# Kernel tuning notes

Measured on AMD Instinct MI355X. Metric: run time of the kernel, lower is better.

## Reference

```python
import jax, jax.numpy as jnp
import numpy as np

B, S, D, F, E = 8, 4096, 512, 2048, 8
INIT_LAMBDA = 0.2
LN_EPS = 1e-5
LN_MERGE = 0.03  # scale used when merging layer_norm expert task-vectors


def setup_inputs() -> dict:
    key = jax.random.key(0)
    ks = jax.random.split(key, 12)
    n = lambda k, shp, s=1.0: jax.random.normal(k, shp, dtype=jnp.float32) * s
    return {
        "hidden_states": n(ks[0], (B, S, D)),
        # DictMoEGate (2 hidden layers): fc1 ~ N(0, 0.01), fc2 bias = init_lambda
        "gfc1_w": n(ks[1], (D, D), 0.01),
        "gfc1_b": jnp.zeros((D,), jnp.float32),
        "gfc2_w": n(ks[2], (E, D), 0.01),
        "gfc2_b": jnp.full((E,), INIT_LAMBDA, dtype=jnp.float32),
        # base PositionWiseFeedForward params (torch Linear layout: [out, in])
        "W1": n(ks[3], (F, D), 0.02),
        "b1": jnp.zeros((F,), jnp.float32),
        "W2": n(ks[4], (D, F), 0.02),
        "b2": jnp.zeros((D,), jnp.float32),
        "ln_g": jnp.ones((D,), jnp.float32),
        "ln_b": jnp.zeros((D,), jnp.float32),
        # expert task vectors (expert_sd - base_sd), one per base param
        "tv_W1": n(ks[5], (E, F, D), 0.02),
        "tv_b1": n(ks[6], (E, F), 0.02),
        "tv_W2": n(ks[7], (E, D, F), 0.02),
        "tv_b2": n(ks[8], (E, D), 0.02),
        "tv_ln_g": n(ks[9], (E, D), 0.02),
        "tv_ln_b": n(ks[10], (E, D), 0.02),
    }


def reference(hidden_states, gfc1_w, gfc1_b, gfc2_w, gfc2_b,
              W1, b1, W2, b2, ln_g, ln_b,
              tv_W1, tv_b1, tv_W2, tv_b2, tv_ln_g, tv_ln_b):
    x = hidden_states  # [B, S, D] (batch_first)
    # --- gate: per-token 2-layer MLP, then mean over sequence -> [B, E] ---
    gh = jax.nn.relu(jnp.einsum('bsd,hd->bsh', x, gfc1_w) + gfc1_b)
    g = (jnp.einsum('bsh,eh->bse', gh, gfc2_w) + gfc2_b).mean(axis=1)  # [B, E]
    # --- per-sample merged weights: base + sum_e g[b,e] * task_vector[e] ---
    W1m = W1 + jnp.einsum('be,efd->bfd', g, tv_W1)   # [B, F, D]
    b1m = b1 + g @ tv_b1                              # [B, F]
    W2m = W2 + jnp.einsum('be,edf->bdf', g, tv_W2)   # [B, D, F]
    b2m = b2 + g @ tv_b2                              # [B, D]
    # layer_norm params: sd = param + sum_e (tv_e - param) * 0.03 (gate-independent)
    lng = ln_g + LN_MERGE * (tv_ln_g - ln_g).sum(axis=0)  # [D]
    lnb = ln_b + LN_MERGE * (tv_ln_b - ln_b).sum(axis=0)  # [D]
    # --- PositionWiseFeedForward with per-sample weights (dropout = eval/identity) ---
    h = jax.nn.relu(jnp.einsum('bsd,bfd->bsf', x, W1m) + b1m[:, None, :])  # [B, S, F]
    out = jnp.einsum('bsf,bdf->bsd', h, W2m) + b2m[:, None, :]             # [B, S, D]
    res = x + out
    mu = res.mean(axis=-1, keepdims=True)
    var = res.var(axis=-1, keepdims=True)
    return (res - mu) * jax.lax.rsqrt(var + LN_EPS) * lng + lnb
```

## Files before the change

kernel.cpp:

```cpp
#include <hip/hip_runtime.h>

typedef __bf16 bf16;
typedef __attribute__((ext_vector_type(4))) __bf16 bf16x4;
typedef __attribute__((ext_vector_type(8))) __bf16 bf16x8;
typedef __attribute__((ext_vector_type(4))) float f32x4;

#define LDS16(gp, lp)                                                          \
  __builtin_amdgcn_global_load_lds(                                            \
      (const __attribute__((address_space(1))) void*)(gp),                     \
      (__attribute__((address_space(3))) void*)(lp), 16, 0, 0)

__global__ __launch_bounds__(256) void prep_kernel(const float* __restrict__ x,
                                                   const float* __restrict__ g1w,
                                                   bf16* __restrict__ x_bf,
                                                   bf16* __restrict__ g1w_bf,
                                                   float* __restrict__ ghsum) {
  const int bid = blockIdx.x;
  if (bid < 8320) {
    const float* src = bid < 8192 ? x : g1w;
    bf16* dst = bid < 8192 ? x_bf : g1w_bf;
    const int base = bid < 8192 ? bid : bid - 8192;
    int i = (base * 256 + threadIdx.x) * 8;
    float4 a = *(const float4*)(src + i);
    float4 b = *(const float4*)(src + i + 4);
    bf16x8 v;
    v[0] = (bf16)a.x; v[1] = (bf16)a.y; v[2] = (bf16)a.z; v[3] = (bf16)a.w;
    v[4] = (bf16)b.x; v[5] = (bf16)b.y; v[6] = (bf16)b.z; v[7] = (bf16)b.w;
    *(bf16x8*)(dst + i) = v;
  } else {
    float4 z = make_float4(0.f, 0.f, 0.f, 0.f);
    float* p = ghsum + threadIdx.x * 16;
#pragma unroll
    for (int k = 0; k < 4; ++k) *(float4*)(p + k * 4) = z;
  }
}

template <int MODE, int KTILES>
__global__ __launch_bounds__(256) void gemm_bt(const bf16* __restrict__ A,
                                               const bf16* __restrict__ B0, long bstride,
                                               const float* __restrict__ bias, long biasStride,
                                               const float* __restrict__ resid,
                                               float* __restrict__ fout,
                                               bf16* __restrict__ hout) {
  constexpr int K = KTILES * 64;
  __shared__ bf16 smem[2 * 128 * 64];
  bf16* As = smem;
  bf16* Bs = smem + 8192;
  const int tid = threadIdx.x;
  const int lane = tid & 63, wv = tid >> 6;
  const int wm = wv >> 1, wn = wv & 1;
  const int lr = lane & 15, q = lane >> 4;
  const int b = blockIdx.z;
  const long blockM = (long)b * 4096 + (long)blockIdx.x * 128;
  const int blockN = blockIdx.y * 128;
  const bf16* Bp = B0 + (long)b * bstride;

  f32x4 acc[4][4] = {};

  const bf16* Ab = A + blockM * K;
  const bf16* Bb = Bp + (long)blockN * K;
  const int srow = lane >> 3;
  const int scol = ((lane & 7) ^ srow) * 8;

  for (int it = 0; it < KTILES; ++it) {
    const int k0 = it * 64;
#pragma unroll
    for (int c = 0; c < 4; ++c) {
      int n = wv * 4 + c;
      int row = n * 8 + srow;
      LDS16(Ab + (long)row * K + k0 + scol, &As[n * 512]);
      LDS16(Bb + (long)row * K + k0 + scol, &Bs[n * 512]);
    }
    __syncthreads();
#pragma unroll
    for (int ks = 0; ks < 2; ++ks) {
      const int c0 = ks * 4 + q;
      const int sw = lane & 7;
      bf16x8 af[4], bfr[4];
#pragma unroll
      for (int i = 0; i < 4; ++i)
        af[i] = *(const bf16x8*)&As[(wm * 64 + i * 16 + lr) * 64 + ((c0 ^ sw) * 8)];
#pragma unroll
      for (int j = 0; j < 4; ++j)
        bfr[j] = *(const bf16x8*)&Bs[(wn * 64 + j * 16 + lr) * 64 + ((c0 ^ sw) * 8)];
#pragma unroll
      for (int i = 0; i < 4; ++i)
#pragma unroll
        for (int j = 0; j < 4; ++j)
          acc[i][j] = __builtin_amdgcn_mfma_f32_16x16x32_bf16(af[i], bfr[j], acc[i][j], 0, 0, 0);
    }
    __syncthreads();
  }

  if (MODE == 0) {
#pragma unroll
    for (int j = 0; j < 4; ++j) {
      const int gc = blockN + wn * 64 + j * 16 + lr;
      const float bv = bias[gc];
      float s = 0.f;
#pragma unroll
      for (int i = 0; i < 4; ++i)
#pragma unroll
        for (int r = 0; r < 4; ++r) {
          float v = acc[i][j][r] + bv;
          s += v > 0.f ? v : 0.f;
        }
      s += __shfl_xor(s, 16);
      s += __shfl_xor(s, 32);
      if (q == 0) atomicAdd(&fout[b * 512 + gc], s);
    }
  } else if (MODE == 1) {
#pragma unroll
    for (int j = 0; j < 4; ++j) {
      const int gc = wn * 64 + j * 16 + lr;
      const float bv = bias[(long)b * biasStride + blockN + gc];
#pragma unroll
      for (int i = 0; i < 4; ++i)
#pragma unroll
        for (int r = 0; r < 4; ++r) {
          const int lrow = wm * 64 + i * 16 + q * 4 + r;
          float v = acc[i][j][r] + bv;
          smem[lrow * 128 + gc] = (bf16)(v > 0.f ? v : 0.f);
        }
    }
    __syncthreads();
#pragma unroll
    for (int p = 0; p < 8; ++p) {
      const int row = p * 16 + (tid >> 4);
      const int col = (tid & 15) * 8;
      *(bf16x8*)&hout[(blockM + row) * 2048 + blockN + col] =
          *(const bf16x8*)&smem[row * 128 + col];
    }
  } else {
#pragma unroll
    for (int j = 0; j < 4; ++j) {
      const int gc = blockN + wn * 64 + j * 16 + lr;
      const float bv = bias[(long)b * biasStride + gc];
#pragma unroll
      for (int i = 0; i < 4; ++i)
#pragma unroll
        for (int r = 0; r < 4; ++r) {
          const long gr = blockM + wm * 64 + i * 16 + q * 4 + r;
          fout[gr * 512 + gc] = acc[i][j][r] + bv + resid[gr * 512 + gc];
        }
    }
  }
}

__global__ __launch_bounds__(512) void small_kernel(
    const float* __restrict__ ghsum, const float* __restrict__ g2w,
    const float* __restrict__ g2b, const float* __restrict__ lngI,
    const float* __restrict__ lnbI, const float* __restrict__ tvlg,
    const float* __restrict__ tvlb, const float* __restrict__ b1,
    const float* __restrict__ tvb1, const float* __restrict__ b2,
    const float* __restrict__ tvb2, float* __restrict__ g, float* __restrict__ lng,
    float* __restrict__ lnb, float* __restrict__ b1m, float* __restrict__ b2m) {
  __shared__ float gs[64];
  const int t = threadIdx.x;
  if (t < 64) {
    const int b = t >> 3, e = t & 7;
    float s = 0.f;
    for (int h = 0; h < 512; ++h) s += ghsum[b * 512 + h] * g2w[e * 512 + h];
    float gv = s * (1.f / 4096.f) + g2b[e];
    gs[t] = gv;
    g[t] = gv;
  }
  __syncthreads();
  if (t < 512) {
    float lg = lngI[t], lb = lnbI[t], sg = 0.f, sb = 0.f;
    for (int e = 0; e < 8; ++e) { sg += tvlg[e * 512 + t]; sb += tvlb[e * 512 + t]; }
    lng[t] = lg + 0.03f * (sg - 8.f * lg);
    lnb[t] = lb + 0.03f * (sb - 8.f * lb);
  }
  for (int i = t; i < 8 * 2048; i += 512) {
    const int b = i >> 11, f = i & 2047;
    float s = b1[f];
    for (int e = 0; e < 8; ++e) s += gs[b * 8 + e] * tvb1[e * 2048 + f];
    b1m[i] = s;
  }
  for (int i = t; i < 8 * 512; i += 512) {
    const int b = i >> 9, d = i & 511;
    float s = b2[d];
    for (int e = 0; e < 8; ++e) s += gs[b * 8 + e] * tvb2[e * 512 + d];
    b2m[i] = s;
  }
}

__global__ __launch_bounds__(256) void merge_kernel(
    const float* __restrict__ W1, const float* __restrict__ tvW1,
    const float* __restrict__ W2, const float* __restrict__ tvW2,
    const float* __restrict__ g, bf16* __restrict__ W1m, bf16* __restrict__ W2m) {
  int idx = (blockIdx.x * 256 + threadIdx.x) * 4;
  const float* Wp;
  const float* tvp;
  bf16* outp;
  if (idx < 1048576) {
    Wp = W1; tvp = tvW1; outp = W1m;
  } else {
    idx -= 1048576;
    Wp = W2; tvp = tvW2; outp = W2m;
  }
  float4 w = *(const float4*)(Wp + idx);
  float4 tv[8];
#pragma unroll
  for (int e = 0; e < 8; ++e) tv[e] = *(const float4*)(tvp + (long)e * 1048576 + idx);
#pragma unroll
  for (int b = 0; b < 8; ++b) {
    float4 s = w;
#pragma unroll
    for (int e = 0; e < 8; ++e) {
      const float ge = g[b * 8 + e];
      s.x += ge * tv[e].x; s.y += ge * tv[e].y;
      s.z += ge * tv[e].z; s.w += ge * tv[e].w;
    }
    bf16x4 o;
    o[0] = (bf16)s.x; o[1] = (bf16)s.y; o[2] = (bf16)s.z; o[3] = (bf16)s.w;
    *(bf16x4*)(outp + (long)b * 1048576 + idx) = o;
  }
}

__global__ __launch_bounds__(256) void ln_kernel(float* __restrict__ out,
                                                 const float* __restrict__ lng,
                                                 const float* __restrict__ lnb) {
  const int wv = threadIdx.x >> 6, lane = threadIdx.x & 63;
  const long row = (long)blockIdx.x * 4 + wv;
  float* p = out + row * 512 + lane * 8;
  float4 a = *(float4*)p;
  float4 b = *(float4*)(p + 4);
  float v[8] = {a.x, a.y, a.z, a.w, b.x, b.y, b.z, b.w};
  float s1 = 0.f, s2 = 0.f;
#pragma unroll
  for (int k = 0; k < 8; ++k) { s1 += v[k]; s2 += v[k] * v[k]; }
#pragma unroll
  for (int off = 32; off > 0; off >>= 1) {
    s1 += __shfl_xor(s1, off);
    s2 += __shfl_xor(s2, off);
  }
  const float mean = s1 * (1.f / 512.f);
  const float var = s2 * (1.f / 512.f) - mean * mean;
  const float rstd = rsqrtf(var + 1e-5f);
  const int c = lane * 8;
  float o[8];
#pragma unroll
  for (int k = 0; k < 8; ++k) o[k] = (v[k] - mean) * rstd * lng[c + k] + lnb[c + k];
  *(float4*)p = make_float4(o[0], o[1], o[2], o[3]);
  *(float4*)(p + 4) = make_float4(o[4], o[5], o[6], o[7]);
}

extern "C" void kernel_launch(void* const* d_in, const int* in_sizes, int n_in,
                              void* d_out, int out_size, void* d_ws, size_t ws_size,
                              hipStream_t stream) {
  const float* x    = (const float*)d_in[0];
  const float* g1w  = (const float*)d_in[1];
  const float* g1b  = (const float*)d_in[2];
  const float* g2w  = (const float*)d_in[3];
  const float* g2b  = (const float*)d_in[4];
  const float* W1   = (const float*)d_in[5];
  const float* b1   = (const float*)d_in[6];
  const float* W2   = (const float*)d_in[7];
  const float* b2   = (const float*)d_in[8];
  const float* lngI = (const float*)d_in[9];
  const float* lnbI = (const float*)d_in[10];
  const float* tvW1 = (const float*)d_in[11];
  const float* tvb1 = (const float*)d_in[12];
  const float* tvW2 = (const float*)d_in[13];
  const float* tvb2 = (const float*)d_in[14];
  const float* tvlg = (const float*)d_in[15];
  const float* tvlb = (const float*)d_in[16];
  float* out = (float*)d_out;

  char* w = (char*)d_ws;
  bf16*  x_bf   = (bf16*)(w);
  bf16*  g1w_bf = (bf16*)(w + 33554432);
  bf16*  W1m    = (bf16*)(w + 34078720);
  bf16*  W2m    = (bf16*)(w + 50855936);
  bf16*  h      = (bf16*)(w + 67633152);
  float* ghsum  = (float*)(w + 201850880);
  float* g      = (float*)(w + 201867264);
  float* b1m    = (float*)(w + 201867520);
  float* b2m    = (float*)(w + 201933056);
  float* lng    = (float*)(w + 201949440);
  float* lnb    = (float*)(w + 201951488);

  prep_kernel<<<8321, 256, 0, stream>>>(x, g1w, x_bf, g1w_bf, ghsum);
  gemm_bt<0, 8><<<dim3(32, 4, 8), 256, 0, stream>>>(x_bf, g1w_bf, 0, g1b, 0,
                                                    nullptr, ghsum, nullptr);
  small_kernel<<<1, 512, 0, stream>>>(ghsum, g2w, g2b, lngI, lnbI, tvlg, tvlb,
                                      b1, tvb1, b2, tvb2, g, lng, lnb, b1m, b2m);
  merge_kernel<<<2048, 256, 0, stream>>>(W1, tvW1, W2, tvW2, g, W1m, W2m);
  gemm_bt<1, 8><<<dim3(32, 16, 8), 256, 0, stream>>>(x_bf, W1m, 1048576, b1m, 2048,
                                                     nullptr, nullptr, h);
  gemm_bt<2, 32><<<dim3(32, 4, 8), 256, 0, stream>>>(h, W2m, 1048576, b2m, 512,
                                                     x, out, nullptr);
  ln_kernel<<<8192, 256, 0, stream>>>(out, lng, lnb);
}
```

Before: 486.6 us.

## Use 256x256 block tiles with double-buffered LDS in bf16 GEMMs

Replaces the 128x128, 4-wave GEMM with a 256x256 tile on 8 waves, a K-step of 32 and a double-buffered LDS pipeline. The next tile's global-to-LDS load is issued before the current tile's MFMAs, so one barrier per iteration replaces two. The goal is more data reuse per load and load/compute overlap. The trade-offs are fewer blocks (256 for the gate and W2 GEMMs, which may underfill the CUs), 128 accumulator registers per lane, and a two-pass epilogue for the h store.

After: 456.3 us. 6.2% less time.

```diff
diff --git a/kernel.cpp b/kernel.cpp
--- a/kernel.cpp
+++ b/kernel.cpp
@@ -35,60 +35,64 @@
   }
 }
 
-template <int MODE, int KTILES>
-__global__ __launch_bounds__(256) void gemm_bt(const bf16* __restrict__ A,
+template <int MODE, int NT>
+__global__ __launch_bounds__(512) void gemm256(const bf16* __restrict__ A,
                                                const bf16* __restrict__ B0, long bstride,
                                                const float* __restrict__ bias, long biasStride,
                                                const float* __restrict__ resid,
                                                float* __restrict__ fout,
                                                bf16* __restrict__ hout) {
-  constexpr int K = KTILES * 64;
-  __shared__ bf16 smem[2 * 128 * 64];
-  bf16* As = smem;
-  bf16* Bs = smem + 8192;
+  constexpr int K = NT * 32;
+  __shared__ __align__(16) bf16 smem[2 * 16384];
   const int tid = threadIdx.x;
   const int lane = tid & 63, wv = tid >> 6;
-  const int wm = wv >> 1, wn = wv & 1;
+  const int wm = wv >> 2, wn = wv & 3;
   const int lr = lane & 15, q = lane >> 4;
   const int b = blockIdx.z;
-  const long blockM = (long)b * 4096 + (long)blockIdx.x * 128;
-  const int blockN = blockIdx.y * 128;
-  const bf16* Bp = B0 + (long)b * bstride;
-
-  f32x4 acc[4][4] = {};
-
+  const long blockM = (long)b * 4096 + (long)blockIdx.x * 256;
+  const int blockN = blockIdx.y * 256;
   const bf16* Ab = A + blockM * K;
-  const bf16* Bb = Bp + (long)blockN * K;
-  const int srow = lane >> 3;
-  const int scol = ((lane & 7) ^ srow) * 8;
-
-  for (int it = 0; it < KTILES; ++it) {
-    const int k0 = it * 64;
-#pragma unroll
-    for (int c = 0; c < 4; ++c) {
-      int n = wv * 4 + c;
-      int row = n * 8 + srow;
-      LDS16(Ab + (long)row * K + k0 + scol, &As[n * 512]);
-      LDS16(Bb + (long)row * K + k0 + scol, &Bs[n * 512]);
-    }
-    __syncthreads();
-#pragma unroll
-    for (int ks = 0; ks < 2; ++ks) {
-      const int c0 = ks * 4 + q;
-      const int sw = lane & 7;
-      bf16x8 af[4], bfr[4];
-#pragma unroll
-      for (int i = 0; i < 4; ++i)
-        af[i] = *(const bf16x8*)&As[(wm * 64 + i * 16 + lr) * 64 + ((c0 ^ sw) * 8)];
+  const bf16* Bb = B0 + (long)b * bstride + (long)blockN * K;
+
+  const int s4 = lane >> 2;
+  const int cch = ((lane & 3) ^ ((s4 >> 1) & 3)) * 8;
+  const int gA0 = wv * 2;
+  const int qa = q ^ ((lr >> 1) & 3);
+  const int aoff = (wm * 128 + lr) * 32 + qa * 8;
+  const int boff = (wn * 64 + lr) * 32 + qa * 8;
+
+  f32x4 acc[8][4] = {};
+
+  auto stage = [&](int t) {
+    bf16* As = smem + (t & 1) * 16384;
+    bf16* Bs = As + 8192;
+    const long k0 = (long)t * 32;
+#pragma unroll
+    for (int li = 0; li < 2; ++li) {
+      const int g = gA0 + li;
+      LDS16(Ab + (long)(g * 16 + s4) * K + k0 + cch, As + g * 512);
+      LDS16(Bb + (long)(g * 16 + s4) * K + k0 + cch, Bs + g * 512);
+    }
+  };
+
+  stage(0);
+  __syncthreads();
+
+#pragma unroll 1
+  for (int t = 0; t < NT; ++t) {
+    if (t + 1 < NT) stage(t + 1);
+    const bf16* As = smem + (t & 1) * 16384;
+    const bf16* Bs = As + 8192;
+    bf16x8 af[8], bfr[4];
+#pragma unroll
+    for (int j = 0; j < 4; ++j) bfr[j] = *(const bf16x8*)&Bs[boff + j * 512];
+#pragma unroll
+    for (int i = 0; i < 8; ++i) af[i] = *(const bf16x8*)&As[aoff + i * 512];
+#pragma unroll
+    for (int i = 0; i < 8; ++i)
 #pragma unroll
       for (int j = 0; j < 4; ++j)
-        bfr[j] = *(const bf16x8*)&Bs[(wn * 64 + j * 16 + lr) * 64 + ((c0 ^ sw) * 8)];
-#pragma unroll
-      for (int i = 0; i < 4; ++i)
-#pragma unroll
-        for (int j = 0; j < 4; ++j)
-          acc[i][j] = __builtin_amdgcn_mfma_f32_16x16x32_bf16(af[i], bfr[j], acc[i][j], 0, 0, 0);
-    }
+        acc[i][j] = __builtin_amdgcn_mfma_f32_16x16x32_bf16(af[i], bfr[j], acc[i][j], 0, 0, 0);
     __syncthreads();
   }
 
@@ -99,7 +103,7 @@
       const float bv = bias[gc];
       float s = 0.f;
 #pragma unroll
-      for (int i = 0; i < 4; ++i)
+      for (int i = 0; i < 8; ++i)
 #pragma unroll
         for (int r = 0; r < 4; ++r) {
           float v = acc[i][j][r] + bv;
@@ -110,26 +114,34 @@
       if (q == 0) atomicAdd(&fout[b * 512 + gc], s);
     }
   } else if (MODE == 1) {
-#pragma unroll
-    for (int j = 0; j < 4; ++j) {
-      const int gc = wn * 64 + j * 16 + lr;
-      const float bv = bias[(long)b * biasStride + blockN + gc];
-#pragma unroll
-      for (int i = 0; i < 4; ++i)
-#pragma unroll
-        for (int r = 0; r < 4; ++r) {
-          const int lrow = wm * 64 + i * 16 + q * 4 + r;
-          float v = acc[i][j][r] + bv;
-          smem[lrow * 128 + gc] = (bf16)(v > 0.f ? v : 0.f);
-        }
-    }
-    __syncthreads();
-#pragma unroll
-    for (int p = 0; p < 8; ++p) {
-      const int row = p * 16 + (tid >> 4);
-      const int col = (tid & 15) * 8;
-      *(bf16x8*)&hout[(blockM + row) * 2048 + blockN + col] =
-          *(const bf16x8*)&smem[row * 128 + col];
+    float bvv[4];
+#pragma unroll
+    for (int j = 0; j < 4; ++j)
+      bvv[j] = bias[(long)b * biasStride + blockN + wn * 64 + j * 16 + lr];
+#pragma unroll 1
+    for (int half = 0; half < 2; ++half) {
+      __syncthreads();
+      if (wm == half) {
+#pragma unroll
+        for (int i = 0; i < 8; ++i)
+#pragma unroll
+          for (int j = 0; j < 4; ++j)
+#pragma unroll
+            for (int r = 0; r < 4; ++r) {
+              const int row = i * 16 + q * 4 + r;
+              const int col = wn * 64 + j * 16 + lr;
+              float v = acc[i][j][r] + bvv[j];
+              smem[row * 256 + col] = (bf16)(v > 0.f ? v : 0.f);
+            }
+      }
+      __syncthreads();
+#pragma unroll
+      for (int p = 0; p < 8; ++p) {
+        const int row = p * 16 + (tid >> 5);
+        const int seg = tid & 31;
+        *(bf16x8*)&hout[(blockM + half * 128 + row) * 2048 + blockN + seg * 8] =
+            *(const bf16x8*)&smem[row * 256 + seg * 8];
+      }
     }
   } else {
 #pragma unroll
@@ -137,10 +149,10 @@
       const int gc = blockN + wn * 64 + j * 16 + lr;
       const float bv = bias[(long)b * biasStride + gc];
 #pragma unroll
-      for (int i = 0; i < 4; ++i)
+      for (int i = 0; i < 8; ++i)
 #pragma unroll
         for (int r = 0; r < 4; ++r) {
-          const long gr = blockM + wm * 64 + i * 16 + q * 4 + r;
+          const long gr = blockM + wm * 128 + i * 16 + q * 4 + r;
           fout[gr * 512 + gc] = acc[i][j][r] + bv + resid[gr * 512 + gc];
         }
     }
@@ -283,14 +295,14 @@
   float* lnb    = (float*)(w + 201951488);
 
   prep_kernel<<<8321, 256, 0, stream>>>(x, g1w, x_bf, g1w_bf, ghsum);
-  gemm_bt<0, 8><<<dim3(32, 4, 8), 256, 0, stream>>>(x_bf, g1w_bf, 0, g1b, 0,
-                                                    nullptr, ghsum, nullptr);
+  gemm256<0, 16><<<dim3(16, 2, 8), 512, 0, stream>>>(x_bf, g1w_bf, 0, g1b, 0,
+                                                     nullptr, ghsum, nullptr);
   small_kernel<<<1, 512, 0, stream>>>(ghsum, g2w, g2b, lngI, lnbI, tvlg, tvlb,
                                       b1, tvb1, b2, tvb2, g, lng, lnb, b1m, b2m);
   merge_kernel<<<2048, 256, 0, stream>>>(W1, tvW1, W2, tvW2, g, W1m, W2m);
-  gemm_bt<1, 8><<<dim3(32, 16, 8), 256, 0, stream>>>(x_bf, W1m, 1048576, b1m, 2048,
+  gemm256<1, 16><<<dim3(16, 8, 8), 512, 0, stream>>>(x_bf, W1m, 1048576, b1m, 2048,
                                                      nullptr, nullptr, h);
-  gemm_bt<2, 32><<<dim3(32, 4, 8), 256, 0, stream>>>(h, W2m, 1048576, b2m, 512,
+  gemm256<2, 64><<<dim3(16, 2, 8), 512, 0, stream>>>(h, W2m, 1048576, b2m, 512,
                                                      x, out, nullptr);
   ln_kernel<<<8192, 256, 0, stream>>>(out, lng, lnb);
 }
```

## Double-buffer GEMM LDS tiles and remap grid to 1D batch-interleaved order

Applied to the files above, without the earlier changes.

The GEMM kernel now keeps two LDS buffers and issues the global-to-LDS loads for the next K tile before computing on the current one, so memory latency can overlap with MFMA work. The launch grid is flattened to 1D, with the batch index in the low bits, so adjacent blocks belong to different batches. LDS use doubles to 64KB per block, which may lower occupancy. Correctness depends on the loop still ending with a barrier before the buffer being overwritten is reused (that part is not shown).

Measured after the change: 476.0 us. 2.2% less time.

```diff
diff --git a/kernel.cpp b/kernel.cpp
--- a/kernel.cpp
+++ b/kernel.cpp
@@ -43,27 +43,29 @@
                                                float* __restrict__ fout,
                                                bf16* __restrict__ hout) {
   constexpr int K = KTILES * 64;
-  __shared__ bf16 smem[2 * 128 * 64];
-  bf16* As = smem;
-  bf16* Bs = smem + 8192;
+  __shared__ __align__(16) bf16 smem[2 * 16384];
   const int tid = threadIdx.x;
   const int lane = tid & 63, wv = tid >> 6;
   const int wm = wv >> 1, wn = wv & 1;
   const int lr = lane & 15, q = lane >> 4;
-  const int b = blockIdx.z;
-  const long blockM = (long)b * 4096 + (long)blockIdx.x * 128;
-  const int blockN = blockIdx.y * 128;
-  const bf16* Bp = B0 + (long)b * bstride;
-
-  f32x4 acc[4][4] = {};
-
+  const int bid = blockIdx.x;
+  const int b = bid & 7;
+  const int rr = bid >> 3;
+  const int mb = rr & 31;
+  const int nb = rr >> 5;
+  const long blockM = (long)b * 4096 + (long)mb * 128;
+  const int blockN = nb * 128;
   const bf16* Ab = A + blockM * K;
-  const bf16* Bb = Bp + (long)blockN * K;
+  const bf16* Bb = B0 + (long)b * bstride + (long)blockN * K;
   const int srow = lane >> 3;
   const int scol = ((lane & 7) ^ srow) * 8;
 
-  for (int it = 0; it < KTILES; ++it) {
-    const int k0 = it * 64;
+  f32x4 acc[4][4] = {};
+
+  auto stage = [&](int it) {
+    bf16* As = smem + (it & 1) * 16384;
+    bf16* Bs = As + 8192;
+    const long k0 = (long)it * 64;
 #pragma unroll
     for (int c = 0; c < 4; ++c) {
       int n = wv * 4 + c;
@@ -71,7 +73,16 @@
       LDS16(Ab + (long)row * K + k0 + scol, &As[n * 512]);
       LDS16(Bb + (long)row * K + k0 + scol, &Bs[n * 512]);
     }
-    __syncthreads();
+  };
+
+  stage(0);
+  __syncthreads();
+
+#pragma unroll 1
+  for (int it = 0; it < KTILES; ++it) {
+    if (it + 1 < KTILES) stage(it + 1);
+    const bf16* As = smem + (it & 1) * 16384;
+    const bf16* Bs = As + 8192;
 #pragma unroll
     for (int ks = 0; ks < 2; ++ks) {
       const int c0 = ks * 4 + q;
@@ -283,14 +294,14 @@
   float* lnb    = (float*)(w + 201951488);
 
   prep_kernel<<<8321, 256, 0, stream>>>(x, g1w, x_bf, g1w_bf, ghsum);
-  gemm_bt<0, 8><<<dim3(32, 4, 8), 256, 0, stream>>>(x_bf, g1w_bf, 0, g1b, 0,
-                                                    nullptr, ghsum, nullptr);
+  gemm_bt<0, 8><<<1024, 256, 0, stream>>>(x_bf, g1w_bf, 0, g1b, 0,
+                                          nullptr, ghsum, nullptr);
   small_kernel<<<1, 512, 0, stream>>>(ghsum, g2w, g2b, lngI, lnbI, tvlg, tvlb,
                                       b1, tvb1, b2, tvb2, g, lng, lnb, b1m, b2m);
   merge_kernel<<<2048, 256, 0, stream>>>(W1, tvW1, W2, tvW2, g, W1m, W2m);
-  gemm_bt<1, 8><<<dim3(32, 16, 8), 256, 0, stream>>>(x_bf, W1m, 1048576, b1m, 2048,
-                                                     nullptr, nullptr, h);
-  gemm_bt<2, 32><<<dim3(32, 4, 8), 256, 0, stream>>>(h, W2m, 1048576, b2m, 512,
-                                                     x, out, nullptr);
+  gemm_bt<1, 8><<<4096, 256, 0, stream>>>(x_bf, W1m, 1048576, b1m, 2048,
+                                          nullptr, nullptr, h);
+  gemm_bt<2, 32><<<1024, 256, 0, stream>>>(h, W2m, 1048576, b2m, 512,
+                                           x, out, nullptr);
   ln_kernel<<<8192, 256, 0, stream>>>(out, lng, lnb);
 }
```
